# Optimization experiments

Hardware: AMD Instinct MI355X
Metric: run time of the kernel (lower is better)

## Reference

```python
import jax, jax.numpy as jnp
import numpy as np

B, H, N, C = 4, 8, 2048, 32
N_SCALAR, N_VEC = 16, 4  # attn_reps = '16x0n+4x1n' -> C = 16 + 4*4 = 32
ETA = jnp.array([1.0, -1.0, -1.0, -1.0], dtype=jnp.float32)  # Minkowski metric diag


def _frame_transform(x, M):
    """Apply per-particle 4x4 matrix M to the vector channels of x.

    x: (B, H, N, C) with layout [16 scalars | 4 four-vectors]
    M: (B, N, 4, 4), shared across heads (module repeats frames over heads).
    """
    s = x[..., :N_SCALAR]                                   # (B,H,N,16) untouched
    v = x[..., N_SCALAR:].reshape(x.shape[:-1] + (N_VEC, 4))  # (B,H,N,4,4)
    v = jnp.einsum('bnij,bhnvj->bhnvi', M, v)
    return jnp.concatenate([s, v.reshape(x.shape[:-1] + (N_VEC * 4,))], axis=-1)


def setup_inputs() -> dict:
    key = jax.random.key(0)
    kq, kk, kv, kf = jax.random.split(key, 4)
    q = jax.random.normal(kq, (B, H, N, C), dtype=jnp.float32)
    k = jax.random.normal(kk, (B, H, N, C), dtype=jnp.float32)
    v = jax.random.normal(kv, (B, H, N, C), dtype=jnp.float32)
    # Genuine Lorentz frames: identity time component + random spatial rotation.
    A = jax.random.normal(kf, (B, N, 3, 3), dtype=jnp.float32)
    Q, _ = jnp.linalg.qr(A)  # (B,N,3,3) orthogonal
    frames = jnp.zeros((B, N, 4, 4), dtype=jnp.float32)
    frames = frames.at[..., 0, 0].set(1.0).at[..., 1:, 1:].set(Q)
    return {'q_local': q, 'k_local': k, 'v_local': v, 'frames': frames}


def reference(q_local, k_local, v_local, frames):
    # Inverse Lorentz frame: L^{-1} = eta L^T eta ; index-lowered inverse = L^T.
    frames_T = jnp.swapaxes(frames, -1, -2)                 # (B,N,4,4)
    inv = frames_T * ETA[:, None] * ETA[None, :]            # eta L^T eta
    lower_inv = frames_T
    # 1) local -> global frame
    q_g = _frame_transform(q_local, inv)
    k_g = _frame_transform(k_local, lower_inv)
    v_g = _frame_transform(v_local, inv)
    # 2) muP-scaled attention (1/d, not 1/sqrt(d))
    scores = jnp.einsum('bhqc,bhkc->bhqk', q_g, k_g) * (1.0 / C)
    weights = jax.nn.softmax(scores, axis=-1)
    out_g = jnp.einsum('bhqk,bhkc->bhqc', weights, v_g)
    # 3) global -> local frame
    return _frame_transform(out_g, frames)
```

## Files before the change

### kernel.cpp

```cpp
#include <hip/hip_runtime.h>
#include <hip/hip_bf16.h>


#define NB 4
#define NH 8
#define NS 2048
#define NC 32

typedef float f32x4 __attribute__((ext_vector_type(4)));
typedef short s16x8 __attribute__((ext_vector_type(8)));
typedef short s16x4 __attribute__((ext_vector_type(4)));

#define QSCALE 0.04511260931463978f

__device__ __forceinline__ short f2bf(float f) {
  union { float f; unsigned u; } c; c.f = f;
  return (short)((c.u + 0x7FFFu + ((c.u >> 16) & 1u)) >> 16);
}

__device__ __forceinline__ void load_Q3(const float* __restrict__ F, int b, int n,
                                        float q9[9]) {
  const float* p = F + ((size_t)(b * NS + n)) * 16 + 5;
  q9[0] = p[0]; q9[1] = p[1]; q9[2] = p[2];
  q9[3] = p[4]; q9[4] = p[5]; q9[5] = p[6];
  q9[6] = p[8]; q9[7] = p[9]; q9[8] = p[10];
}

__device__ __forceinline__ void rotT(const float q9[9], f32x4& v) {
  const float x = v[1], y = v[2], z = v[3];
  v[1] = q9[0] * x + q9[3] * y + q9[6] * z;
  v[2] = q9[1] * x + q9[4] * y + q9[7] * z;
  v[3] = q9[2] * x + q9[5] * y + q9[8] * z;
}

__device__ __forceinline__ void rotF(const float q9[9], f32x4& v) {
  const float x = v[1], y = v[2], z = v[3];
  v[1] = q9[0] * x + q9[1] * y + q9[2] * z;
  v[2] = q9[3] * x + q9[4] * y + q9[5] * z;
  v[3] = q9[6] * x + q9[7] * y + q9[8] * z;
}

__launch_bounds__(256)
__global__ void rot_cast(const float* __restrict__ Kg,
                         const float* __restrict__ Vg,
                         const float* __restrict__ Fg,
                         unsigned short* __restrict__ Kbf,
                         unsigned short* __restrict__ Vt) {
  const int gid = blockIdx.x * 256 + threadIdx.x;
  if (gid < 65536) {
    const int r = gid;
    const int n = r & (NS - 1);
    const int b = r >> 14;
    const float* p = Kg + (size_t)r * NC;
    f32x4 c[8];
#pragma unroll
    for (int i = 0; i < 8; i++) c[i] = *(const f32x4*)(p + 4 * i);
    float q9[9]; load_Q3(Fg, b, n, q9);
#pragma unroll
    for (int i = 4; i < 8; i++) rotT(q9, c[i]);
    unsigned short* o = Kbf + (size_t)r * NC;
#pragma unroll
    for (int i = 0; i < 8; i += 2) {
      s16x8 w;
#pragma unroll
      for (int e = 0; e < 4; e++) {
        w[e]     = f2bf(c[i][e]);
        w[4 + e] = f2bf(c[i + 1][e]);
      }
      *(s16x8*)(o + 4 * i) = w;
    }
  } else {
    const int r  = gid - 65536;
    const int bh = r >> 9;
    const int b  = bh >> 3;
    const int K0 = (r & 511) << 2;
    const float* vsrc = Vg + ((size_t)bh * NS + K0) * NC;
    s16x4 outc[32];
#pragma unroll
    for (int k = 0; k < 4; k++) {
      f32x4 c[8];
#pragma unroll
      for (int i = 0; i < 8; i++) c[i] = *(const f32x4*)(vsrc + (size_t)k * NC + 4 * i);
      float q9[9]; load_Q3(Fg, b, K0 + k, q9);
#pragma unroll
      for (int i = 4; i < 8; i++) rotT(q9, c[i]);
#pragma unroll
      for (int i = 0; i < 8; i++)
#pragma unroll
        for (int e = 0; e < 4; e++) outc[i * 4 + e][k] = f2bf(c[i][e]);
    }
    const int cg     = K0 & 31;
    const int sub4   = cg >> 2;
    const int newsub = (sub4 & 3) * 2 + (sub4 >> 2);
    const int pos    = ((K0 & 127) >> 5) * 32 + newsub * 4;
    unsigned short* o = Vt + (size_t)bh * (NS * NC) + ((K0 >> 7) & 15) * 4096 + pos;
#pragma unroll
    for (int ch = 0; ch < 32; ch++) *(s16x4*)(o + ch * 128) = outc[ch];
  }
}

__launch_bounds__(256, 2)
__global__ void lloca_attn(const float* __restrict__ Qg,
                           const unsigned short* __restrict__ Kbf,
                           const unsigned short* __restrict__ Vt,
                           const float* __restrict__ Fg,
                           float* __restrict__ Og) {
  __shared__ __align__(16) unsigned short Klds[2][128 * 40];
  __shared__ __align__(16) unsigned short Vlds[2][32 * 136];

  const int tid  = threadIdx.x;
  const int lane = tid & 63;
  const int wv   = tid >> 6;
  const int g    = lane >> 4;
  const int lq   = lane & 15;

  const int blk = blockIdx.x;
  const int b   = blk >> 7;
  const int h   = (blk >> 4) & 7;
  const int qb  = blk & 15;

  const size_t bhr = (size_t)(b * NH + h) * NS;
  const unsigned short* Kp  = Kbf + bhr * NC;
  const unsigned short* Vtp = Vt  + bhr * NC;
  float*                Op  = Og  + bhr * NC;

  const int qbase = qb * 128 + wv * 32;

  const f32x4 zero4 = {0.f, 0.f, 0.f, 0.f};
  const short ONE = (short)0x3F80;
  const s16x8 ones8 = {ONE, ONE, ONE, ONE, ONE, ONE, ONE, ONE};

  s16x8 qfrag[2];
  f32x4 acc[2][2];
  f32x4 accL[2];
#pragma unroll
  for (int t = 0; t < 2; t++) {
    const int qi = qbase + t * 16 + lq;
    const float* qp = Qg + (bhr + qi) * NC + g * 8;
    f32x4 a = *(const f32x4*)qp;
    f32x4 c = *(const f32x4*)(qp + 4);
    if (g >= 2) {
      float q9[9]; load_Q3(Fg, b, qi, q9);
      rotT(q9, a);
      rotT(q9, c);
    }
#pragma unroll
    for (int e = 0; e < 4; e++) {
      qfrag[t][e]     = f2bf(a[e] * QSCALE);
      qfrag[t][4 + e] = f2bf(c[e] * QSCALE);
    }
    acc[t][0] = zero4;
    acc[t][1] = zero4;
    accL[t]   = zero4;
  }

  const int key = tid >> 1, h2 = tid & 1;
  const unsigned short* kbase = Kp + (size_t)key * NC + h2 * 16;
  const unsigned short* vbase = Vtp + tid * 16;
  const int vrow = tid >> 3, vc8 = tid & 7;
  const int vdst = vrow * 136 + vc8 * 16;

  s16x8 rk0, rk1, rv0, rv1;

  rk0 = *(const s16x8*)kbase;
  rk1 = *(const s16x8*)(kbase + 8);
  rv0 = *(const s16x8*)vbase;
  rv1 = *(const s16x8*)(vbase + 8);

#define WRITE_TILE(buf)                                                        \
  do {                                                                         \
    *(s16x8*)&Klds[buf][key * 40 + h2 * 16]     = rk0;                         \
    *(s16x8*)&Klds[buf][key * 40 + h2 * 16 + 8] = rk1;                         \
    *(s16x8*)&Vlds[buf][vdst]                   = rv0;                         \
    *(s16x8*)&Vlds[buf][vdst + 8]               = rv1;                         \
  } while (0)

  WRITE_TILE(0);
  __syncthreads();

  const int NT = NS / 128;
  for (int i = 0; i < NT; i++) {
    const int cur = i & 1;
    if (i + 1 < NT) {
      const size_t koff = (size_t)(i + 1) * 128 * NC;
      rk0 = *(const s16x8*)(kbase + koff);
      rk1 = *(const s16x8*)(kbase + koff + 8);
      rv0 = *(const s16x8*)(vbase + koff);
      rv1 = *(const s16x8*)(vbase + koff + 8);
    }
#pragma unroll
    for (int kgi = 0; kgi < 4; kgi++) {
      const int kgb = kgi * 32;
      const s16x8 kf0 = *(const s16x8*)&Klds[cur][(kgb + lq) * 40 + g * 8];
      const s16x8 kf1 = *(const s16x8*)&Klds[cur][(kgb + 16 + lq) * 40 + g * 8];
      const s16x8 va0 = *(const s16x8*)&Vlds[cur][lq * 136 + kgb + g * 8];
      const s16x8 va1 = *(const s16x8*)&Vlds[cur][(16 + lq) * 136 + kgb + g * 8];
#pragma unroll
      for (int t = 0; t < 2; t++) {
        f32x4 s0 = __builtin_amdgcn_mfma_f32_16x16x32_bf16(kf0, qfrag[t], zero4, 0, 0, 0);
        f32x4 s1 = __builtin_amdgcn_mfma_f32_16x16x32_bf16(kf1, qfrag[t], zero4, 0, 0, 0);
        float p0 = __builtin_amdgcn_exp2f(s0[0]);
        float p1 = __builtin_amdgcn_exp2f(s0[1]);
        float p2 = __builtin_amdgcn_exp2f(s0[2]);
        float p3 = __builtin_amdgcn_exp2f(s0[3]);
        float p4 = __builtin_amdgcn_exp2f(s1[0]);
        float p5 = __builtin_amdgcn_exp2f(s1[1]);
        float p6 = __builtin_amdgcn_exp2f(s1[2]);
        float p7 = __builtin_amdgcn_exp2f(s1[3]);
        union { __hip_bfloat162 h2v[4]; s16x8 v; } pk;
        pk.h2v[0] = __float22bfloat162_rn(make_float2(p0, p1));
        pk.h2v[1] = __float22bfloat162_rn(make_float2(p2, p3));
        pk.h2v[2] = __float22bfloat162_rn(make_float2(p4, p5));
        pk.h2v[3] = __float22bfloat162_rn(make_float2(p6, p7));
        accL[t]   = __builtin_amdgcn_mfma_f32_16x16x32_bf16(ones8, pk.v, accL[t], 0, 0, 0);
        acc[t][0] = __builtin_amdgcn_mfma_f32_16x16x32_bf16(va0,   pk.v, acc[t][0], 0, 0, 0);
        acc[t][1] = __builtin_amdgcn_mfma_f32_16x16x32_bf16(va1,   pk.v, acc[t][1], 0, 0, 0);
      }
    }
    __syncthreads();
    if (i + 1 < NT) {
      WRITE_TILE(cur ^ 1);
      __syncthreads();
    }
  }

#pragma unroll
  for (int t = 0; t < 2; t++) {
    const float inv = 1.0f / accL[t][0];
    const int qi = qbase + t * 16 + lq;
    float* op = Op + (size_t)qi * NC;
    f32x4 o0, o1;
#pragma unroll
    for (int r = 0; r < 4; r++) {
      o0[r] = acc[t][0][r] * inv;
      o1[r] = acc[t][1][r] * inv;
    }
    float q9[9]; load_Q3(Fg, b, qi, q9);
    rotF(q9, o1);
    *(f32x4*)(op + g * 4)      = o0;
    *(f32x4*)(op + 16 + g * 4) = o1;
  }
}

extern "C" void kernel_launch(void* const* d_in, const int* in_sizes, int n_in,
                              void* d_out, int out_size, void* d_ws, size_t ws_size,
                              hipStream_t stream) {
  (void)in_sizes; (void)n_in; (void)ws_size; (void)out_size;
  const float* q = (const float*)d_in[0];
  const float* k = (const float*)d_in[1];
  const float* v = (const float*)d_in[2];
  const float* f = (const float*)d_in[3];
  float* o = (float*)d_out;

  const size_t NEL = (size_t)NB * NH * NS * NC;
  unsigned short* kbf = (unsigned short*)d_ws;
  unsigned short* vt  = kbf + NEL;

  hipLaunchKernelGGL(rot_cast, dim3(320), dim3(256), 0, stream,
                     k, v, f, kbf, vt);
  hipLaunchKernelGGL(lloca_attn, dim3(512), dim3(256), 0, stream,
                     q, kbf, vt, f, o);
}
```

Baseline: 44.70 us.

## Use 512-thread blocks with one 16-query tile per wave and 256-key LDS tiles

Each block now runs 8 waves, and each wave owns a single 16-query tile instead of two. K/V tiles staged in LDS grow to 256 keys so all 512 threads load one chunk each, which halves the number of barrier rounds. Wave priority is raised around the MFMA/exp loop with s_setprio. The aim is more waves in flight to hide latency and fewer syncs, at the cost of no K/V fragment reuse across query tiles within a wave and doubled LDS per block.

```diff
diff --git a/kernel.cpp b/kernel.cpp
--- a/kernel.cpp
+++ b/kernel.cpp
@@ -99,14 +99,14 @@
   }
 }
 
-__launch_bounds__(256, 2)
+__launch_bounds__(512, 4)
 __global__ void lloca_attn(const float* __restrict__ Qg,
                            const unsigned short* __restrict__ Kbf,
                            const unsigned short* __restrict__ Vt,
                            const float* __restrict__ Fg,
                            float* __restrict__ Og) {
-  __shared__ __align__(16) unsigned short Klds[2][128 * 40];
-  __shared__ __align__(16) unsigned short Vlds[2][32 * 136];
+  __shared__ __align__(16) unsigned short Klds[2][256 * 40];
+  __shared__ __align__(16) unsigned short Vlds[2][32 * 264];
 
   const int tid  = threadIdx.x;
   const int lane = tid & 63;
@@ -124,18 +124,14 @@
   const unsigned short* Vtp = Vt  + bhr * NC;
   float*                Op  = Og  + bhr * NC;
 
-  const int qbase = qb * 128 + wv * 32;
+  const int qi = qb * 128 + wv * 16 + lq;
 
   const f32x4 zero4 = {0.f, 0.f, 0.f, 0.f};
   const short ONE = (short)0x3F80;
   const s16x8 ones8 = {ONE, ONE, ONE, ONE, ONE, ONE, ONE, ONE};
 
-  s16x8 qfrag[2];
-  f32x4 acc[2][2];
-  f32x4 accL[2];
-#pragma unroll
-  for (int t = 0; t < 2; t++) {
-    const int qi = qbase + t * 16 + lq;
+  s16x8 qfrag;
+  {
     const float* qp = Qg + (bhr + qi) * NC + g * 8;
     f32x4 a = *(const f32x4*)qp;
     f32x4 c = *(const f32x4*)(qp + 4);
@@ -146,19 +142,18 @@
     }
 #pragma unroll
     for (int e = 0; e < 4; e++) {
-      qfrag[t][e]     = f2bf(a[e] * QSCALE);
-      qfrag[t][4 + e] = f2bf(c[e] * QSCALE);
-    }
-    acc[t][0] = zero4;
-    acc[t][1] = zero4;
-    accL[t]   = zero4;
-  }
+      qfrag[e]     = f2bf(a[e] * QSCALE);
+      qfrag[4 + e] = f2bf(c[e] * QSCALE);
+    }
+  }
+
+  f32x4 acc0 = zero4, acc1 = zero4, accL = zero4;
 
   const int key = tid >> 1, h2 = tid & 1;
   const unsigned short* kbase = Kp + (size_t)key * NC + h2 * 16;
   const unsigned short* vbase = Vtp + tid * 16;
-  const int vrow = tid >> 3, vc8 = tid & 7;
-  const int vdst = vrow * 136 + vc8 * 16;
+  const int kdst = key * 40 + h2 * 16;
+  const int vdst = ((tid >> 3) & 31) * 264 + (tid >> 8) * 128 + (tid & 7) * 16;
 
   s16x8 rk0, rk1, rv0, rv1;
 
@@ -169,71 +164,68 @@
 
 #define WRITE_TILE(buf)                                                        \
   do {                                                                         \
-    *(s16x8*)&Klds[buf][key * 40 + h2 * 16]     = rk0;                         \
-    *(s16x8*)&Klds[buf][key * 40 + h2 * 16 + 8] = rk1;                         \
-    *(s16x8*)&Vlds[buf][vdst]                   = rv0;                         \
-    *(s16x8*)&Vlds[buf][vdst + 8]               = rv1;                         \
+    *(s16x8*)&Klds[buf][kdst]     = rk0;                                       \
+    *(s16x8*)&Klds[buf][kdst + 8] = rk1;                                       \
+    *(s16x8*)&Vlds[buf][vdst]     = rv0;                                       \
+    *(s16x8*)&Vlds[buf][vdst + 8] = rv1;                                       \
   } while (0)
 
   WRITE_TILE(0);
   __syncthreads();
 
-  const int NT = NS / 128;
-  for (int i = 0; i < NT; i++) {
+  const int NTT = NS / 256;
+  for (int i = 0; i < NTT; i++) {
     const int cur = i & 1;
-    if (i + 1 < NT) {
-      const size_t koff = (size_t)(i + 1) * 128 * NC;
-      rk0 = *(const s16x8*)(kbase + koff);
-      rk1 = *(const s16x8*)(kbase + koff + 8);
-      rv0 = *(const s16x8*)(vbase + koff);
-      rv1 = *(const s16x8*)(vbase + koff + 8);
-    }
-#pragma unroll
-    for (int kgi = 0; kgi < 4; kgi++) {
+    if (i + 1 < NTT) {
+      const size_t off = (size_t)(i + 1) * 8192;
+      rk0 = *(const s16x8*)(kbase + off);
+      rk1 = *(const s16x8*)(kbase + off + 8);
+      rv0 = *(const s16x8*)(vbase + off);
+      rv1 = *(const s16x8*)(vbase + off + 8);
+    }
+    __builtin_amdgcn_s_setprio(1);
+#pragma unroll
+    for (int kgi = 0; kgi < 8; kgi++) {
       const int kgb = kgi * 32;
       const s16x8 kf0 = *(const s16x8*)&Klds[cur][(kgb + lq) * 40 + g * 8];
       const s16x8 kf1 = *(const s16x8*)&Klds[cur][(kgb + 16 + lq) * 40 + g * 8];
-      const s16x8 va0 = *(const s16x8*)&Vlds[cur][lq * 136 + kgb + g * 8];
-      const s16x8 va1 = *(const s16x8*)&Vlds[cur][(16 + lq) * 136 + kgb + g * 8];
-#pragma unroll
-      for (int t = 0; t < 2; t++) {
-        f32x4 s0 = __builtin_amdgcn_mfma_f32_16x16x32_bf16(kf0, qfrag[t], zero4, 0, 0, 0);
-        f32x4 s1 = __builtin_amdgcn_mfma_f32_16x16x32_bf16(kf1, qfrag[t], zero4, 0, 0, 0);
-        float p0 = __builtin_amdgcn_exp2f(s0[0]);
-        float p1 = __builtin_amdgcn_exp2f(s0[1]);
-        float p2 = __builtin_amdgcn_exp2f(s0[2]);
-        float p3 = __builtin_amdgcn_exp2f(s0[3]);
-        float p4 = __builtin_amdgcn_exp2f(s1[0]);
-        float p5 = __builtin_amdgcn_exp2f(s1[1]);
-        float p6 = __builtin_amdgcn_exp2f(s1[2]);
-        float p7 = __builtin_amdgcn_exp2f(s1[3]);
-        union { __hip_bfloat162 h2v[4]; s16x8 v; } pk;
-        pk.h2v[0] = __float22bfloat162_rn(make_float2(p0, p1));
-        pk.h2v[1] = __float22bfloat162_rn(make_float2(p2, p3));
-        pk.h2v[2] = __float22bfloat162_rn(make_float2(p4, p5));
-        pk.h2v[3] = __float22bfloat162_rn(make_float2(p6, p7));
-        accL[t]   = __builtin_amdgcn_mfma_f32_16x16x32_bf16(ones8, pk.v, accL[t], 0, 0, 0);
-        acc[t][0] = __builtin_amdgcn_mfma_f32_16x16x32_bf16(va0,   pk.v, acc[t][0], 0, 0, 0);
-        acc[t][1] = __builtin_amdgcn_mfma_f32_16x16x32_bf16(va1,   pk.v, acc[t][1], 0, 0, 0);
-      }
-    }
+      const s16x8 va0 = *(const s16x8*)&Vlds[cur][lq * 264 + kgb + g * 8];
+      const s16x8 va1 = *(const s16x8*)&Vlds[cur][(16 + lq) * 264 + kgb + g * 8];
+      f32x4 s0 = __builtin_amdgcn_mfma_f32_16x16x32_bf16(kf0, qfrag, zero4, 0, 0, 0);
+      f32x4 s1 = __builtin_amdgcn_mfma_f32_16x16x32_bf16(kf1, qfrag, zero4, 0, 0, 0);
+      float p0 = __builtin_amdgcn_exp2f(s0[0]);
+      float p1 = __builtin_amdgcn_exp2f(s0[1]);
+      float p2 = __builtin_amdgcn_exp2f(s0[2]);
+      float p3 = __builtin_amdgcn_exp2f(s0[3]);
+      float p4 = __builtin_amdgcn_exp2f(s1[0]);
+      float p5 = __builtin_amdgcn_exp2f(s1[1]);
+      float p6 = __builtin_amdgcn_exp2f(s1[2]);
+      float p7 = __builtin_amdgcn_exp2f(s1[3]);
+      union { __hip_bfloat162 h2v[4]; s16x8 v; } pk;
+      pk.h2v[0] = __float22bfloat162_rn(make_float2(p0, p1));
+      pk.h2v[1] = __float22bfloat162_rn(make_float2(p2, p3));
+      pk.h2v[2] = __float22bfloat162_rn(make_float2(p4, p5));
+      pk.h2v[3] = __float22bfloat162_rn(make_float2(p6, p7));
+      accL = __builtin_amdgcn_mfma_f32_16x16x32_bf16(ones8, pk.v, accL, 0, 0, 0);
+      acc0 = __builtin_amdgcn_mfma_f32_16x16x32_bf16(va0,   pk.v, acc0, 0, 0, 0);
+      acc1 = __builtin_amdgcn_mfma_f32_16x16x32_bf16(va1,   pk.v, acc1, 0, 0, 0);
+    }
+    __builtin_amdgcn_s_setprio(0);
     __syncthreads();
-    if (i + 1 < NT) {
+    if (i + 1 < NTT) {
       WRITE_TILE(cur ^ 1);
       __syncthreads();
     }
   }
 
-#pragma unroll
-  for (int t = 0; t < 2; t++) {
-    const float inv = 1.0f / accL[t][0];
-    const int qi = qbase + t * 16 + lq;
+  {
+    const float inv = 1.0f / accL[0];
     float* op = Op + (size_t)qi * NC;
     f32x4 o0, o1;
 #pragma unroll
     for (int r = 0; r < 4; r++) {
-      o0[r] = acc[t][0][r] * inv;
-      o1[r] = acc[t][1][r] * inv;
+      o0[r] = acc0[r] * inv;
+      o1[r] = acc1[r] * inv;
     }
     float q9[9]; load_Q3(Fg, b, qi, q9);
     rotF(q9, o1);
@@ -258,6 +250,6 @@
 
   hipLaunchKernelGGL(rot_cast, dim3(320), dim3(256), 0, stream,
                      k, v, f, kbf, vt);
-  hipLaunchKernelGGL(lloca_attn, dim3(512), dim3(256), 0, stream,
+  hipLaunchKernelGGL(lloca_attn, dim3(512), dim3(512), 0, stream,
                      q, kbf, vt, f, o);
 }
```

Result: no change. 45.35 us (+1.5%).

## Load K/V MFMA fragments directly from global memory, drop LDS staging

Applied to the files above, without the earlier changes.

Removes the shared-memory double-buffered K/V tiles and the block-level barriers; each wave now reads its MFMA fragments straight from global memory (L2/L1) with a two-deep register prefetch. Block indices are also remapped so consecutive blocks are spread across batch-heads (an XCD-aware swizzle), which is meant to improve L2 locality per die. This gives up cooperative reuse: every wave re-reads the same K/V from cache, so global/L1 traffic rises fourfold per block, and latency hiding now relies on the register prefetch alone.

```diff
diff --git a/kernel.cpp b/kernel.cpp
--- a/kernel.cpp
+++ b/kernel.cpp
@@ -105,24 +105,22 @@
                            const unsigned short* __restrict__ Vt,
                            const float* __restrict__ Fg,
                            float* __restrict__ Og) {
-  __shared__ __align__(16) unsigned short Klds[2][128 * 40];
-  __shared__ __align__(16) unsigned short Vlds[2][32 * 136];
-
   const int tid  = threadIdx.x;
   const int lane = tid & 63;
   const int wv   = tid >> 6;
   const int g    = lane >> 4;
   const int lq   = lane & 15;
 
-  const int blk = blockIdx.x;
-  const int b   = blk >> 7;
-  const int h   = (blk >> 4) & 7;
-  const int qb  = blk & 15;
-
-  const size_t bhr = (size_t)(b * NH + h) * NS;
-  const unsigned short* Kp  = Kbf + bhr * NC;
-  const unsigned short* Vtp = Vt  + bhr * NC;
-  float*                Op  = Og  + bhr * NC;
+  const int bid  = blockIdx.x;
+  const int work = (bid & 7) * 64 + (bid >> 3);
+  const int bh   = work >> 4;
+  const int qb   = work & 15;
+  const int b    = bh >> 3;
+
+  const size_t bhr = (size_t)bh * NS;
+  const unsigned short* Kp = Kbf + bhr * NC;
+  const unsigned short* Vp = Vt  + bhr * NC;
+  float*                Op = Og  + bhr * NC;
 
   const int qbase = qb * 128 + wv * 32;
 
@@ -136,7 +134,7 @@
 #pragma unroll
   for (int t = 0; t < 2; t++) {
     const int qi = qbase + t * 16 + lq;
-    const float* qp = Qg + (bhr + qi) * NC + g * 8;
+    const float* qp = Qg + ((size_t)(bhr + qi)) * NC + g * 8;
     f32x4 a = *(const f32x4*)qp;
     f32x4 c = *(const f32x4*)(qp + 4);
     if (g >= 2) {
@@ -154,74 +152,52 @@
     accL[t]   = zero4;
   }
 
-  const int key = tid >> 1, h2 = tid & 1;
-  const unsigned short* kbase = Kp + (size_t)key * NC + h2 * 16;
-  const unsigned short* vbase = Vtp + tid * 16;
-  const int vrow = tid >> 3, vc8 = tid & 7;
-  const int vdst = vrow * 136 + vc8 * 16;
-
-  s16x8 rk0, rk1, rv0, rv1;
-
-  rk0 = *(const s16x8*)kbase;
-  rk1 = *(const s16x8*)(kbase + 8);
-  rv0 = *(const s16x8*)vbase;
-  rv1 = *(const s16x8*)(vbase + 8);
-
-#define WRITE_TILE(buf)                                                        \
+  const int koff = lq * 32 + g * 8;
+  const int voff = lq * 128 + g * 8;
+
+#define LOADF(kgb, kf0, kf1, va0, va1)                                         \
   do {                                                                         \
-    *(s16x8*)&Klds[buf][key * 40 + h2 * 16]     = rk0;                         \
-    *(s16x8*)&Klds[buf][key * 40 + h2 * 16 + 8] = rk1;                         \
-    *(s16x8*)&Vlds[buf][vdst]                   = rv0;                         \
-    *(s16x8*)&Vlds[buf][vdst + 8]               = rv1;                         \
+    const unsigned short* ka = Kp + (kgb) * 32 + koff;                         \
+    const unsigned short* va =                                                 \
+        Vp + (((kgb) >> 7) << 12) + ((kgb) & 127) + voff;                      \
+    kf0 = *(const s16x8*)ka;                                                   \
+    kf1 = *(const s16x8*)(ka + 512);                                           \
+    va0 = *(const s16x8*)va;                                                   \
+    va1 = *(const s16x8*)(va + 2048);                                          \
   } while (0)
 
-  WRITE_TILE(0);
-  __syncthreads();
-
-  const int NT = NS / 128;
-  for (int i = 0; i < NT; i++) {
-    const int cur = i & 1;
-    if (i + 1 < NT) {
-      const size_t koff = (size_t)(i + 1) * 128 * NC;
-      rk0 = *(const s16x8*)(kbase + koff);
-      rk1 = *(const s16x8*)(kbase + koff + 8);
-      rv0 = *(const s16x8*)(vbase + koff);
-      rv1 = *(const s16x8*)(vbase + koff + 8);
-    }
-#pragma unroll
-    for (int kgi = 0; kgi < 4; kgi++) {
-      const int kgb = kgi * 32;
-      const s16x8 kf0 = *(const s16x8*)&Klds[cur][(kgb + lq) * 40 + g * 8];
-      const s16x8 kf1 = *(const s16x8*)&Klds[cur][(kgb + 16 + lq) * 40 + g * 8];
-      const s16x8 va0 = *(const s16x8*)&Vlds[cur][lq * 136 + kgb + g * 8];
-      const s16x8 va1 = *(const s16x8*)&Vlds[cur][(16 + lq) * 136 + kgb + g * 8];
-#pragma unroll
-      for (int t = 0; t < 2; t++) {
-        f32x4 s0 = __builtin_amdgcn_mfma_f32_16x16x32_bf16(kf0, qfrag[t], zero4, 0, 0, 0);
-        f32x4 s1 = __builtin_amdgcn_mfma_f32_16x16x32_bf16(kf1, qfrag[t], zero4, 0, 0, 0);
-        float p0 = __builtin_amdgcn_exp2f(s0[0]);
-        float p1 = __builtin_amdgcn_exp2f(s0[1]);
-        float p2 = __builtin_amdgcn_exp2f(s0[2]);
-        float p3 = __builtin_amdgcn_exp2f(s0[3]);
-        float p4 = __builtin_amdgcn_exp2f(s1[0]);
-        float p5 = __builtin_amdgcn_exp2f(s1[1]);
-        float p6 = __builtin_amdgcn_exp2f(s1[2]);
-        float p7 = __builtin_amdgcn_exp2f(s1[3]);
-        union { __hip_bfloat162 h2v[4]; s16x8 v; } pk;
-        pk.h2v[0] = __float22bfloat162_rn(make_float2(p0, p1));
-        pk.h2v[1] = __float22bfloat162_rn(make_float2(p2, p3));
-        pk.h2v[2] = __float22bfloat162_rn(make_float2(p4, p5));
-        pk.h2v[3] = __float22bfloat162_rn(make_float2(p6, p7));
-        accL[t]   = __builtin_amdgcn_mfma_f32_16x16x32_bf16(ones8, pk.v, accL[t], 0, 0, 0);
-        acc[t][0] = __builtin_amdgcn_mfma_f32_16x16x32_bf16(va0,   pk.v, acc[t][0], 0, 0, 0);
-        acc[t][1] = __builtin_amdgcn_mfma_f32_16x16x32_bf16(va1,   pk.v, acc[t][1], 0, 0, 0);
-      }
-    }
-    __syncthreads();
-    if (i + 1 < NT) {
-      WRITE_TILE(cur ^ 1);
-      __syncthreads();
-    }
+#define COMPUTEF(kf0, kf1, va0, va1)                                           \
+  do {                                                                         \
+    _Pragma("unroll")                                                          \
+    for (int t = 0; t < 2; t++) {                                              \
+      f32x4 s0 = __builtin_amdgcn_mfma_f32_16x16x32_bf16(kf0, qfrag[t], zero4, 0, 0, 0); \
+      f32x4 s1 = __builtin_amdgcn_mfma_f32_16x16x32_bf16(kf1, qfrag[t], zero4, 0, 0, 0); \
+      float p0 = __builtin_amdgcn_exp2f(s0[0]);                                \
+      float p1 = __builtin_amdgcn_exp2f(s0[1]);                                \
+      float p2 = __builtin_amdgcn_exp2f(s0[2]);                                \
+      float p3 = __builtin_amdgcn_exp2f(s0[3]);                                \
+      float p4 = __builtin_amdgcn_exp2f(s1[0]);                                \
+      float p5 = __builtin_amdgcn_exp2f(s1[1]);                                \
+      float p6 = __builtin_amdgcn_exp2f(s1[2]);                                \
+      float p7 = __builtin_amdgcn_exp2f(s1[3]);                                \
+      union { __hip_bfloat162 h2v[4]; s16x8 v; } pk;                           \
+      pk.h2v[0] = __float22bfloat162_rn(make_float2(p0, p1));                  \
+      pk.h2v[1] = __float22bfloat162_rn(make_float2(p2, p3));                  \
+      pk.h2v[2] = __float22bfloat162_rn(make_float2(p4, p5));                  \
+      pk.h2v[3] = __float22bfloat162_rn(make_float2(p6, p7));                  \
+      accL[t]   = __builtin_amdgcn_mfma_f32_16x16x32_bf16(ones8, pk.v, accL[t], 0, 0, 0); \
+      acc[t][0] = __builtin_amdgcn_mfma_f32_16x16x32_bf16(va0,   pk.v, acc[t][0], 0, 0, 0); \
+      acc[t][1] = __builtin_amdgcn_mfma_f32_16x16x32_bf16(va1,   pk.v, acc[t][1], 0, 0, 0); \
+    }                                                                          \
+  } while (0)
+
+  s16x8 kA0, kA1, vA0, vA1, kB0, kB1, vB0, vB1;
+  LOADF(0, kA0, kA1, vA0, vA1);
+  for (int kg = 0; kg < 64; kg += 2) {
+    LOADF((kg + 1) * 32, kB0, kB1, vB0, vB1);
+    COMPUTEF(kA0, kA1, vA0, vA1);
+    if (kg + 2 < 64) LOADF((kg + 2) * 32, kA0, kA1, vA0, vA1);
+    COMPUTEF(kB0, kB1, vB0, vB1);
   }
 
 #pragma unroll
```

Result: slower. 63.66 us (+42.4%).

## Stage K/V tiles via direct global-to-LDS loads with XOR-swizzled V layout

Applied to the files above, without the earlier changes.

Replaces the register-staged K/V tile copy (global load into VGPRs, then LDS write, then an extra barrier) with global_load_lds 16-byte direct transfers into unpadded LDS buffers. This removes one barrier per tile and frees registers. The V transpose prep kernel now writes an XOR-swizzled layout, so the unpadded V rows avoid LDS bank conflicts when the compute loop reads them with the matching swizzle. It also raises wave priority around the MFMA loop. The risk is that the single remaining barrier must also cover completion of the async loads; if it does not, the next tile may be read before its data has landed, and K reads from the unpadded rows may now hit bank conflicts.

```diff
diff --git a/kernel.cpp b/kernel.cpp
--- a/kernel.cpp
+++ b/kernel.cpp
@@ -16,6 +16,12 @@
 __device__ __forceinline__ short f2bf(float f) {
   union { float f; unsigned u; } c; c.f = f;
   return (short)((c.u + 0x7FFFu + ((c.u >> 16) & 1u)) >> 16);
+}
+
+__device__ __forceinline__ void gload16(const void* g, void* l) {
+  __builtin_amdgcn_global_load_lds(
+      (const __attribute__((address_space(1))) unsigned int*)g,
+      (__attribute__((address_space(3))) unsigned int*)l, 16, 0, 0);
 }
 
 __device__ __forceinline__ void load_Q3(const float* __restrict__ F, int b, int n,
@@ -93,9 +99,12 @@
     const int sub4   = cg >> 2;
     const int newsub = (sub4 & 3) * 2 + (sub4 >> 2);
     const int pos    = ((K0 & 127) >> 5) * 32 + newsub * 4;
-    unsigned short* o = Vt + (size_t)bh * (NS * NC) + ((K0 >> 7) & 15) * 4096 + pos;
-#pragma unroll
-    for (int ch = 0; ch < 32; ch++) *(s16x4*)(o + ch * 128) = outc[ch];
+    const int gpos   = pos >> 3;
+    const int rem    = pos & 7;
+    unsigned short* ob = Vt + (size_t)bh * (NS * NC) + ((K0 >> 7) & 15) * 4096;
+#pragma unroll
+    for (int ch = 0; ch < 32; ch++)
+      *(s16x4*)(ob + ch * 128 + ((gpos ^ (ch & 15)) << 3) + rem) = outc[ch];
   }
 }
 
@@ -105,8 +114,8 @@
                            const unsigned short* __restrict__ Vt,
                            const float* __restrict__ Fg,
                            float* __restrict__ Og) {
-  __shared__ __align__(16) unsigned short Klds[2][128 * 40];
-  __shared__ __align__(16) unsigned short Vlds[2][32 * 136];
+  __shared__ __align__(16) unsigned short Klds[2][128 * 32];
+  __shared__ __align__(16) unsigned short Vlds[2][32 * 128];
 
   const int tid  = threadIdx.x;
   const int lane = tid & 63;
@@ -154,47 +163,35 @@
     accL[t]   = zero4;
   }
 
-  const int key = tid >> 1, h2 = tid & 1;
-  const unsigned short* kbase = Kp + (size_t)key * NC + h2 * 16;
-  const unsigned short* vbase = Vtp + tid * 16;
-  const int vrow = tid >> 3, vc8 = tid & 7;
-  const int vdst = vrow * 136 + vc8 * 16;
-
-  s16x8 rk0, rk1, rv0, rv1;
-
-  rk0 = *(const s16x8*)kbase;
-  rk1 = *(const s16x8*)(kbase + 8);
-  rv0 = *(const s16x8*)vbase;
-  rv1 = *(const s16x8*)(vbase + 8);
-
-#define WRITE_TILE(buf)                                                        \
+  const int sgrp = wv * 2;
+  const int lel  = lane * 8;
+
+#define STAGE(buf, i)                                                          \
   do {                                                                         \
-    *(s16x8*)&Klds[buf][key * 40 + h2 * 16]     = rk0;                         \
-    *(s16x8*)&Klds[buf][key * 40 + h2 * 16 + 8] = rk1;                         \
-    *(s16x8*)&Vlds[buf][vdst]                   = rv0;                         \
-    *(s16x8*)&Vlds[buf][vdst + 8]               = rv1;                         \
+    const unsigned short* ks = Kp + (size_t)(i) * 4096 + sgrp * 512 + lel;     \
+    const unsigned short* vs = Vtp + (size_t)(i) * 4096 + sgrp * 512 + lel;    \
+    gload16(ks,       &Klds[buf][sgrp * 512]);                                 \
+    gload16(ks + 512, &Klds[buf][sgrp * 512 + 512]);                           \
+    gload16(vs,       &Vlds[buf][sgrp * 512]);                                 \
+    gload16(vs + 512, &Vlds[buf][sgrp * 512 + 512]);                           \
   } while (0)
 
-  WRITE_TILE(0);
+  STAGE(0, 0);
   __syncthreads();
 
-  const int NT = NS / 128;
-  for (int i = 0; i < NT; i++) {
+  const int NTT = NS / 128;
+  for (int i = 0; i < NTT; i++) {
     const int cur = i & 1;
-    if (i + 1 < NT) {
-      const size_t koff = (size_t)(i + 1) * 128 * NC;
-      rk0 = *(const s16x8*)(kbase + koff);
-      rk1 = *(const s16x8*)(kbase + koff + 8);
-      rv0 = *(const s16x8*)(vbase + koff);
-      rv1 = *(const s16x8*)(vbase + koff + 8);
-    }
+    if (i + 1 < NTT) STAGE(cur ^ 1, i + 1);
+    __builtin_amdgcn_s_setprio(1);
 #pragma unroll
     for (int kgi = 0; kgi < 4; kgi++) {
       const int kgb = kgi * 32;
-      const s16x8 kf0 = *(const s16x8*)&Klds[cur][(kgb + lq) * 40 + g * 8];
-      const s16x8 kf1 = *(const s16x8*)&Klds[cur][(kgb + 16 + lq) * 40 + g * 8];
-      const s16x8 va0 = *(const s16x8*)&Vlds[cur][lq * 136 + kgb + g * 8];
-      const s16x8 va1 = *(const s16x8*)&Vlds[cur][(16 + lq) * 136 + kgb + g * 8];
+      const s16x8 kf0 = *(const s16x8*)&Klds[cur][(kgb + lq) * 32 + g * 8];
+      const s16x8 kf1 = *(const s16x8*)&Klds[cur][(kgb + 16 + lq) * 32 + g * 8];
+      const int vsw = (((kgb >> 3) + g) ^ lq) << 3;
+      const s16x8 va0 = *(const s16x8*)&Vlds[cur][lq * 128 + vsw];
+      const s16x8 va1 = *(const s16x8*)&Vlds[cur][(16 + lq) * 128 + vsw];
 #pragma unroll
       for (int t = 0; t < 2; t++) {
         f32x4 s0 = __builtin_amdgcn_mfma_f32_16x16x32_bf16(kf0, qfrag[t], zero4, 0, 0, 0);
@@ -217,11 +214,8 @@
         acc[t][1] = __builtin_amdgcn_mfma_f32_16x16x32_bf16(va1,   pk.v, acc[t][1], 0, 0, 0);
       }
     }
+    __builtin_amdgcn_s_setprio(0);
     __syncthreads();
-    if (i + 1 < NT) {
-      WRITE_TILE(cur ^ 1);
-      __syncthreads();
-    }
   }
 
 #pragma unroll
```

Measured after the change: 45.86 us. 2.6% more time.
